# Optimization experiments

Hardware: AMD Instinct MI355X
Metric: run time of the kernel (lower is better)

Reference implementation:

```python
import jax, jax.numpy as jnp
import numpy as np

T, D, H, B = 2048, 1152, 16, 8
DH = D // H  # 72


def _apply_rope(x, cos_h, sin_h):
    # x: [T, H, DH]; cos_h, sin_h: [T, DH//2] (already chunked halves)
    c = jnp.concatenate([cos_h, cos_h], axis=-1)[:, None, :]  # [T,1,DH]
    s = jnp.concatenate([sin_h, sin_h], axis=-1)[:, None, :]
    x1, x2 = jnp.split(x, 2, axis=-1)
    rot = jnp.concatenate([-x2, x1], axis=-1)
    return x * c + rot * s


def setup_inputs() -> dict:
    key = jax.random.key(0)
    ks = jax.random.split(key, 12)
    hidden_states = jax.random.normal(ks[0], (T, D), jnp.float32)
    inner = jnp.sort(jax.random.randint(ks[1], (B - 1,), 1, T))
    cu_seqlens = jnp.concatenate(
        [jnp.zeros((1,), jnp.int32), inner.astype(jnp.int32), jnp.full((1,), T, jnp.int32)])
    cos = jax.random.uniform(ks[2], (T, DH), jnp.float32, -1.0, 1.0)
    sin = jax.random.uniform(ks[3], (T, DH), jnp.float32, -1.0, 1.0)
    std = 0.02
    Wq = jax.random.normal(ks[4], (D, D), jnp.float32) * std
    Wk = jax.random.normal(ks[5], (D, D), jnp.float32) * std
    Wv = jax.random.normal(ks[6], (D, D), jnp.float32) * std
    Wo = jax.random.normal(ks[7], (D, D), jnp.float32) * std
    bq = jnp.zeros((D,), jnp.float32)
    bk = jnp.zeros((D,), jnp.float32)
    bv = jnp.zeros((D,), jnp.float32)
    bo = jnp.zeros((D,), jnp.float32)
    return {"hidden_states": hidden_states, "cu_seqlens": cu_seqlens,
            "cos": cos, "sin": sin,
            "Wq": Wq, "bq": bq, "Wk": Wk, "bk": bk,
            "Wv": Wv, "bv": bv, "Wo": Wo, "bo": bo}


def reference(hidden_states, cu_seqlens, cos, sin, Wq, bq, Wk, bk, Wv, bv, Wo, bo):
    t = hidden_states.shape[0]
    scale = DH ** -0.5
    q = (hidden_states @ Wq.T + bq).reshape(t, H, DH)
    k = (hidden_states @ Wk.T + bk).reshape(t, H, DH)
    v = (hidden_states @ Wv.T + bv).reshape(t, H, DH)
    # RoPE: cos/sin [T, DH] are chunked in half along last dim, first half used
    cos_h = cos[:, : DH // 2]
    sin_h = sin[:, : DH // 2]
    q = _apply_rope(q, cos_h, sin_h)
    k = _apply_rope(k, cos_h, sin_h)
    # segment ids from cu_seqlens -> block-diagonal (varlen) attention mask
    pos = jnp.arange(t)
    seg = jnp.searchsorted(cu_seqlens, pos, side='right') - 1  # [T]
    mask = seg[:, None] == seg[None, :]  # [T, T]
    scores = jnp.einsum('thd,shd->hts', q, k) * scale  # [H, T, T]
    scores = jnp.where(mask[None], scores, jnp.float32(-1e30))
    attn = jax.nn.softmax(scores, axis=-1)
    out = jnp.einsum('hts,shd->thd', attn, v).reshape(t, D)
    return out @ Wo.T + bo
```

## Files before the change

kernel.cpp:

```cpp
#include <hip/hip_runtime.h>

#define TT 2048
#define DM 1152
#define NHEAD 16
#define HDIM 72
#define HDP 96
#define HDV 80
#define KSPLIT 2

typedef __attribute__((ext_vector_type(8))) __bf16 bf16x8;
typedef __attribute__((ext_vector_type(4))) float f32x4;
typedef unsigned short u16;
typedef unsigned int u32;
typedef __attribute__((ext_vector_type(4))) u16 u16x4;

__device__ inline u16 f2bf(float f){
  u32 u = __builtin_bit_cast(u32, f);
  return (u16)((u + 0x7FFFu + ((u >> 16) & 1u)) >> 16);
}
__device__ inline float bf2f(u16 v){
  return __builtin_bit_cast(float, ((u32)v) << 16);
}
__device__ inline bf16x8 ldb8(const u16* p){
  uint4 u = *(const uint4*)p;
  return __builtin_bit_cast(bf16x8, u);
}
__device__ inline f32x4 mfma16(bf16x8 a, bf16x8 b, f32x4 c){
  return __builtin_amdgcn_mfma_f32_16x16x32_bf16(a, b, c, 0, 0, 0);
}
__device__ inline void gload_lds16(const u16* g, u16* l){
  __builtin_amdgcn_global_load_lds(
      (const __attribute__((address_space(1))) void*)g,
      (__attribute__((address_space(3))) void*)l, 16, 0, 0);
}

__global__ void k_convert(const float* hid, const float* wq, const float* wk,
                          const float* wv, const float* wo, const int* cu,
                          u16* hb, u16* wqb, u16* wkb, u16* wvb, u16* wob,
                          u16* qhb, u16* khb, int* seg)
{
  long i = (long)blockIdx.x * blockDim.x + threadIdx.x;
  const long NHID4 = (long)TT * DM / 4;
  const long NW4 = (long)DM * DM / 4;
  const long NC4 = NHID4 + 4*NW4;
  if (i < NC4) {
    const float4* src; u16* dst; long o;
    if (i < NHID4) { src = (const float4*)hid; dst = hb; o = i; }
    else {
      long j = i - NHID4;
      int w = (int)(j / NW4);
      o = j - (long)w * NW4;
      src = (const float4*)((w==0)?wq:(w==1)?wk:(w==2)?wv:wo);
      dst = (w==0)?wqb:(w==1)?wkb:(w==2)?wvb:wob;
    }
    float4 v = src[o];
    u16x4 r; r.x = f2bf(v.x); r.y = f2bf(v.y); r.z = f2bf(v.z); r.w = f2bf(v.w);
    *(u16x4*)(dst + o*4) = r;
  } else {
    long j = i - NC4;
    const long PER = (long)NHEAD*TT*12;
    if (j < 2*PER) {
      int arr = (int)(j / PER);
      long r = j - (long)arr*PER;
      long th = r / 12;
      int c = (int)(r - th*12);
      ((u32*)(arr ? khb : qhb))[th*48 + 36 + c] = 0u;
    }
  }
  if (i < TT) {
    int c = 0;
    for (int e = 0; e < 9; ++e) c += (cu[e] <= (int)i);
    seg[i] = c - 1;
  }
}

__device__ __forceinline__ void gemm_m128n64(const u16* __restrict__ A,
                                             const u16* __restrict__ W,
                                             const float* __restrict__ bias,
                                             void* out, int mode, float oscale)
{
  __shared__ __align__(16) u16 As[2][128*32];
  __shared__ __align__(16) u16 Bs[2][64*32];
  int tid = threadIdx.x;
  int lane = tid & 63, wid = tid >> 6;
  int l15 = lane & 15, quad = lane >> 4;
  int bm = blockIdx.x * 128, bn = blockIdx.y * 64;
  int wm = wid*32;
  f32x4 acc[2][4] = {};
  const u16* ga = A + (long)(bm + (tid>>2))*DM + (tid&3)*8;
  const u16* gb = W + (long)(bn + (tid>>2))*DM + (tid&3)*8;
  {
    u16* lA = As[0] + wid*512; u16* lB = Bs[0] + wid*512;
    gload_lds16(ga,          lA);
    gload_lds16(ga + 64*DM,  lA + 2048);
    gload_lds16(gb,          lB);
  }
  int cur = 0;
  for (int k0 = 0; k0 < DM; k0 += 32, cur ^= 1) {
    __syncthreads();
    if (k0 + 32 < DM) {
      u16* lA = As[cur^1] + wid*512; u16* lB = Bs[cur^1] + wid*512;
      gload_lds16(ga + k0 + 32,          lA);
      gload_lds16(ga + k0 + 32 + 64*DM,  lA + 2048);
      gload_lds16(gb + k0 + 32,          lB);
    }
    bf16x8 af[2], bfr[4];
    for (int i=0;i<2;i++) af[i]  = ldb8(As[cur] + (wm + i*16 + l15)*32 + quad*8);
    for (int i=0;i<4;i++) bfr[i] = ldb8(Bs[cur] + (i*16 + l15)*32 + quad*8);
    for (int mi=0;mi<2;mi++)
      for (int ni=0;ni<4;ni++)
        acc[mi][ni] = mfma16(af[mi], bfr[ni], acc[mi][ni]);
  }
  for (int ni=0;ni<4;ni++){
    int n = bn + ni*16 + l15;
    float bv_ = bias[n];
    int h = n / HDIM, dh = n - (n / HDIM)*HDIM;
    for (int mi=0;mi<2;mi++){
      int m0 = bm + wm + mi*16 + quad*4;
      for (int r=0;r<4;r++){
        float v = (acc[mi][ni][r] + bv_) * oscale;
        int m = m0 + r;
        if (mode == 0) {
          ((u16*)out)[((long)(h*TT + m))*HDP + dh] = f2bf(v);
        } else {
          ((u16*)out)[((long)(h*HDV + dh))*TT + m] = f2bf(v);
        }
      }
    }
  }
}

__global__ __launch_bounds__(256, 4) void k_gemm_qkv(const u16* __restrict__ A,
    const u16* __restrict__ Wq, const u16* __restrict__ Wk, const u16* __restrict__ Wv,
    const float* __restrict__ bq, const float* __restrict__ bk, const float* __restrict__ bv,
    u16* oq, u16* ok, u16* ov)
{
  const float scale = 0.11785113019775793f;
  int z = blockIdx.z;
  if (z == 0)      gemm_m128n64(A, Wq, bq, oq, 0, scale);
  else if (z == 1) gemm_m128n64(A, Wk, bk, ok, 0, 1.0f);
  else             gemm_m128n64(A, Wv, bv, ov, 2, 1.0f);
}

__global__ __launch_bounds__(256, 4) void k_gemm_o(const u16* __restrict__ A,
    const u16* __restrict__ W, const float* __restrict__ bias, float* out)
{
  __shared__ __align__(16) u16 As[2][64*32];
  __shared__ __align__(16) u16 Bs[2][64*32];
  int tid = threadIdx.x;
  int lane = tid & 63, wid = tid >> 6;
  int l15 = lane & 15, quad = lane >> 4;
  int bm = blockIdx.x * 64, bn = blockIdx.y * 64;
  int wm = (wid>>1)*32, wn = (wid&1)*32;
  f32x4 acc[2][2] = {};
  const u16* ga = A + (long)(bm + (tid>>2))*DM + (tid&3)*8;
  const u16* gb = W + (long)(bn + (tid>>2))*DM + (tid&3)*8;
  {
    gload_lds16(ga, As[0] + wid*512);
    gload_lds16(gb, Bs[0] + wid*512);
  }
  int cur = 0;
  for (int k0 = 0; k0 < DM; k0 += 32, cur ^= 1) {
    __syncthreads();
    if (k0 + 32 < DM) {
      gload_lds16(ga + k0 + 32, As[cur^1] + wid*512);
      gload_lds16(gb + k0 + 32, Bs[cur^1] + wid*512);
    }
    bf16x8 af[2], bfr[2];
    for (int i=0;i<2;i++) af[i]  = ldb8(As[cur] + (wm + i*16 + l15)*32 + quad*8);
    for (int i=0;i<2;i++) bfr[i] = ldb8(Bs[cur] + (wn + i*16 + l15)*32 + quad*8);
    for (int mi=0;mi<2;mi++)
      for (int ni=0;ni<2;ni++)
        acc[mi][ni] = mfma16(af[mi], bfr[ni], acc[mi][ni]);
  }
  for (int ni=0;ni<2;ni++){
    int n = bn + wn + ni*16 + l15;
    float bv_ = bias[n];
    for (int mi=0;mi<2;mi++){
      int m0 = bm + wm + mi*16 + quad*4;
      for (int r=0;r<4;r++)
        out[(long)(m0 + r)*DM + n] = acc[mi][ni][r] + bv_;
    }
  }
}

__global__ void k_rope(u16* qh, u16* kh, const float* __restrict__ cosb,
                       const float* __restrict__ sinb)
{
  int i = blockIdx.x * blockDim.x + threadIdx.x;
  const int total = 2 * NHEAD * TT * 36;
  if (i >= total) return;
  int d = i % 36; int rest = i / 36;
  int t = rest % TT; rest /= TT;
  int h = rest % NHEAD; int qk = rest / NHEAD;
  u16* base = (qk ? kh : qh) + ((long)h*TT + t)*HDP;
  float x1 = bf2f(base[d]), x2 = bf2f(base[d+36]);
  float c = cosb[t*HDIM + d], s = sinb[t*HDIM + d];
  base[d]    = f2bf(x1*c - x2*s);
  base[d+36] = f2bf(x2*c + x1*s);
}

__global__ __launch_bounds__(256, 2) void k_attn(const u16* __restrict__ qh,
                                                 const u16* __restrict__ kh,
                                                 const u16* __restrict__ vT,
                                                 const int* __restrict__ seg,
                                                 const int* __restrict__ cu,
                                                 float* __restrict__ pacc,
                                                 float* __restrict__ plsum)
{
  __shared__ __align__(16) u16 pbuf[4][16][144];
  int h = blockIdx.y;
  int z = blockIdx.z;
  int tid = threadIdx.x, lane = tid & 63, wid = tid >> 6;
  int l15 = lane & 15, quad = lane >> 4;
  int qb0 = blockIdx.x * 128;
  int qbase = qb0 + wid*32;

  bf16x8 qf[2][3];
  int lo[2][4], hi[2][4];
  for (int t=0;t<2;t++){
    const u16* qp = qh + ((long)h*TT + qbase + t*16 + l15)*HDP + quad*8;
    qf[t][0] = ldb8(qp); qf[t][1] = ldb8(qp+32); qf[t][2] = ldb8(qp+64);
    for (int r=0;r<4;r++){
      int sq = seg[qbase + t*16 + quad*4 + r];
      lo[t][r] = cu[sq]; hi[t][r] = cu[sq+1];
    }
  }
  f32x4 acc[2][5] = {};
  float lsum[2][4] = {};

  int s_begin = cu[seg[qb0]] & ~63;
  int s_end = cu[seg[qb0 + 127] + 1];
  int nt = (s_end - s_begin + 63) >> 6;
  int nt0 = (nt + 1) >> 1;
  int it_lo = z ? nt0 : 0;
  int it_hi = z ? nt : nt0;

  const u16* kbase = kh + (long)h*TT*HDP;
  const u16* vbase = vT + ((long)h*HDV + l15)*TT + quad*8;

  if (it_lo < it_hi) {
    bf16x8 kf[4][3];
    {
      const u16* kp = kbase + (long)(s_begin + it_lo*64 + l15)*HDP + quad*8;
      for (int j=0;j<4;j++)
        for (int c=0;c<3;c++)
          kf[j][c] = ldb8(kp + j*16*HDP + c*32);
    }
    for (int it = it_lo; it < it_hi; ++it) {
      int s0 = s_begin + it*64;
      f32x4 sc[2][4] = {};
      for (int j=0;j<4;j++){
        sc[0][j] = mfma16(qf[0][0], kf[j][0], sc[0][j]);
        sc[1][j] = mfma16(qf[1][0], kf[j][0], sc[1][j]);
        sc[0][j] = mfma16(qf[0][1], kf[j][1], sc[0][j]);
        sc[1][j] = mfma16(qf[1][1], kf[j][1], sc[1][j]);
        sc[0][j] = mfma16(qf[0][2], kf[j][2], sc[0][j]);
        sc[1][j] = mfma16(qf[1][2], kf[j][2], sc[1][j]);
      }
      const u16* vp = vbase + s0;
      bf16x8 vf[5][2];
      for (int n=0;n<5;n++){
        vf[n][0] = ldb8(vp + (long)n*16*TT);
        vf[n][1] = ldb8(vp + (long)n*16*TT + 32);
      }
      if (it + 1 < it_hi) {
        const u16* kp = kbase + (long)(s0 + 64 + l15)*HDP + quad*8;
        for (int j=0;j<4;j++)
          for (int c=0;c<3;c++)
            kf[j][c] = ldb8(kp + j*16*HDP + c*32);
      }
      for (int t=0;t<2;t++){
        for (int j=0;j<4;j++){
          int kidx = s0 + j*16 + l15;
          for (int r=0;r<4;r++){
            bool in = (kidx >= lo[t][r]) && (kidx < hi[t][r]);
            float p = in ? __expf(sc[t][j][r]) : 0.f;
            lsum[t][r] += p;
            pbuf[wid][quad*4+r][t*72 + j*16 + l15] = f2bf(p);
          }
        }
      }
      bf16x8 pf[2][2];
      for (int t=0;t<2;t++){
        pf[t][0] = ldb8(&pbuf[wid][l15][t*72 + quad*8]);
        pf[t][1] = ldb8(&pbuf[wid][l15][t*72 + 32 + quad*8]);
      }
      for (int n=0;n<5;n++){
        acc[0][n] = mfma16(pf[0][0], vf[n][0], acc[0][n]);
        acc[1][n] = mfma16(pf[1][0], vf[n][0], acc[1][n]);
        acc[0][n] = mfma16(pf[0][1], vf[n][1], acc[0][n]);
        acc[1][n] = mfma16(pf[1][1], vf[n][1], acc[1][n]);
      }
    }
  }
  for (int off=1; off<16; off<<=1)
    for (int t=0;t<2;t++)
      for (int r=0;r<4;r++)
        lsum[t][r] += __shfl_xor(lsum[t][r], off, 64);
  for (int t=0;t<2;t++){
    for (int n=0;n<5;n++){
      int dh = n*16 + l15;
      for (int r=0;r<4;r++){
        int tk = qbase + t*16 + quad*4 + r;
        pacc[(((long)z*TT + tk)*NHEAD + h)*HDV + dh] = acc[t][n][r];
      }
    }
    if (l15 == 0){
      for (int r=0;r<4;r++){
        int tk = qbase + t*16 + quad*4 + r;
        plsum[((long)z*TT + tk)*NHEAD + h] = lsum[t][r];
      }
    }
  }
}

__global__ void k_combine(const float* __restrict__ pacc,
                          const float* __restrict__ plsum,
                          u16* __restrict__ ao)
{
  int i = blockIdx.x*blockDim.x + threadIdx.x;
  const int total = TT*NHEAD*HDIM;
  if (i >= total) return;
  int dh = i % HDIM; int rest = i / HDIM;
  int h = rest % NHEAD; int t = rest / NHEAD;
  long i0 = ((long)t*NHEAD + h)*HDV + dh;
  float a = pacc[i0] + pacc[(long)TT*NHEAD*HDV + i0];
  float l = plsum[t*NHEAD + h] + plsum[TT*NHEAD + t*NHEAD + h];
  ao[(long)t*DM + h*HDIM + dh] = f2bf(a / l);
}

extern "C" void kernel_launch(void* const* d_in, const int* in_sizes, int n_in,
                              void* d_out, int out_size, void* d_ws, size_t ws_size,
                              hipStream_t stream)
{
  const float* hid  = (const float*)d_in[0];
  const int*   cu   = (const int*)d_in[1];
  const float* cosb = (const float*)d_in[2];
  const float* sinb = (const float*)d_in[3];
  const float* wq   = (const float*)d_in[4];
  const float* bq   = (const float*)d_in[5];
  const float* wk   = (const float*)d_in[6];
  const float* bk   = (const float*)d_in[7];
  const float* wv   = (const float*)d_in[8];
  const float* bv   = (const float*)d_in[9];
  const float* wo   = (const float*)d_in[10];
  const float* bo   = (const float*)d_in[11];

  char* ws = (char*)d_ws;
  u16* hb  = (u16*)ws; ws += (long)TT*DM*2;
  u16* wqb = (u16*)ws; ws += (long)DM*DM*2;
  u16* wkb = (u16*)ws; ws += (long)DM*DM*2;
  u16* wvb = (u16*)ws; ws += (long)DM*DM*2;
  u16* wob = (u16*)ws; ws += (long)DM*DM*2;
  u16* qhb = (u16*)ws; ws += (long)NHEAD*TT*HDP*2;
  u16* khb = (u16*)ws; ws += (long)NHEAD*TT*HDP*2;
  u16* vTb = (u16*)ws; ws += (long)NHEAD*HDV*TT*2;
  u16* aob = (u16*)ws; ws += (long)TT*DM*2;
  int* seg = (int*)ws; ws += (long)TT*4;
  float* pacc  = (float*)ws; ws += (long)KSPLIT*TT*NHEAD*HDV*4;
  float* plsum = (float*)ws; ws += (long)KSPLIT*TT*NHEAD*4;

  long nconv = ((long)TT*DM + 4L*DM*DM)/4 + 2L*NHEAD*TT*12;
  k_convert<<<dim3((nconv + 255)/256), 256, 0, stream>>>(
      hid, wq, wk, wv, wo, cu, hb, wqb, wkb, wvb, wob, qhb, khb, seg);

  dim3 gqkv(TT/128, DM/64, 3);
  k_gemm_qkv<<<gqkv, 256, 0, stream>>>(hb, wqb, wkb, wvb, bq, bk, bv, qhb, khb, vTb);

  int nrope = 2*NHEAD*TT*36;
  k_rope<<<dim3((nrope + 255)/256), 256, 0, stream>>>(qhb, khb, cosb, sinb);

  dim3 ga(TT/128, NHEAD, KSPLIT);
  k_attn<<<ga, 256, 0, stream>>>(qhb, khb, vTb, seg, cu, pacc, plsum);

  int ncomb = TT*NHEAD*HDIM;
  k_combine<<<dim3((ncomb + 255)/256), 256, 0, stream>>>(pacc, plsum, aob);

  dim3 go(TT/64, DM/64);
  k_gemm_o<<<go, 256, 0, stream>>>(aob, wob, bo, (float*)d_out);
}
```

Baseline: 195.3 us.

## Fuse split-K attention combine into last-arriving block; reuse 128x64 GEMM for output projection

The separate combine kernel is removed. Each attention block now does a threadfence and an atomic counter increment, and the last split block for a tile sums the partial accumulators and normalizes them into the bf16 attention output. The counters are zeroed inside the rope kernel. The output projection now reuses the shared 128x64 GEMM routine with a new fp32 store mode instead of its own 64x64 kernel. This saves one launch and a pass over the partials, at the cost of atomics and a serialized tail in attention blocks, and it halves the number of output-GEMM blocks.

After: 256.2 us. 31.2% more time.

```diff
diff --git a/kernel.cpp b/kernel.cpp
--- a/kernel.cpp
+++ b/kernel.cpp
@@ -122,8 +122,10 @@
         int m = m0 + r;
         if (mode == 0) {
           ((u16*)out)[((long)(h*TT + m))*HDP + dh] = f2bf(v);
+        } else if (mode == 2) {
+          ((u16*)out)[((long)(h*HDV + dh))*TT + m] = f2bf(v);
         } else {
-          ((u16*)out)[((long)(h*HDV + dh))*TT + m] = f2bf(v);
+          ((float*)out)[(long)m*DM + n] = v;
         }
       }
     }
@@ -145,49 +147,14 @@
 __global__ __launch_bounds__(256, 4) void k_gemm_o(const u16* __restrict__ A,
     const u16* __restrict__ W, const float* __restrict__ bias, float* out)
 {
-  __shared__ __align__(16) u16 As[2][64*32];
-  __shared__ __align__(16) u16 Bs[2][64*32];
-  int tid = threadIdx.x;
-  int lane = tid & 63, wid = tid >> 6;
-  int l15 = lane & 15, quad = lane >> 4;
-  int bm = blockIdx.x * 64, bn = blockIdx.y * 64;
-  int wm = (wid>>1)*32, wn = (wid&1)*32;
-  f32x4 acc[2][2] = {};
-  const u16* ga = A + (long)(bm + (tid>>2))*DM + (tid&3)*8;
-  const u16* gb = W + (long)(bn + (tid>>2))*DM + (tid&3)*8;
-  {
-    gload_lds16(ga, As[0] + wid*512);
-    gload_lds16(gb, Bs[0] + wid*512);
-  }
-  int cur = 0;
-  for (int k0 = 0; k0 < DM; k0 += 32, cur ^= 1) {
-    __syncthreads();
-    if (k0 + 32 < DM) {
-      gload_lds16(ga + k0 + 32, As[cur^1] + wid*512);
-      gload_lds16(gb + k0 + 32, Bs[cur^1] + wid*512);
-    }
-    bf16x8 af[2], bfr[2];
-    for (int i=0;i<2;i++) af[i]  = ldb8(As[cur] + (wm + i*16 + l15)*32 + quad*8);
-    for (int i=0;i<2;i++) bfr[i] = ldb8(Bs[cur] + (wn + i*16 + l15)*32 + quad*8);
-    for (int mi=0;mi<2;mi++)
-      for (int ni=0;ni<2;ni++)
-        acc[mi][ni] = mfma16(af[mi], bfr[ni], acc[mi][ni]);
-  }
-  for (int ni=0;ni<2;ni++){
-    int n = bn + wn + ni*16 + l15;
-    float bv_ = bias[n];
-    for (int mi=0;mi<2;mi++){
-      int m0 = bm + wm + mi*16 + quad*4;
-      for (int r=0;r<4;r++)
-        out[(long)(m0 + r)*DM + n] = acc[mi][ni][r] + bv_;
-    }
-  }
+  gemm_m128n64(A, W, bias, out, 1, 1.0f);
 }
 
 __global__ void k_rope(u16* qh, u16* kh, const float* __restrict__ cosb,
-                       const float* __restrict__ sinb)
+                       const float* __restrict__ sinb, int* done)
 {
   int i = blockIdx.x * blockDim.x + threadIdx.x;
+  if (i < NHEAD*(TT/128)) done[i] = 0;
   const int total = 2 * NHEAD * TT * 36;
   if (i >= total) return;
   int d = i % 36; int rest = i / 36;
@@ -206,9 +173,12 @@
                                                  const int* __restrict__ seg,
                                                  const int* __restrict__ cu,
                                                  float* __restrict__ pacc,
-                                                 float* __restrict__ plsum)
+                                                 float* __restrict__ plsum,
+                                                 int* __restrict__ done,
+                                                 u16* __restrict__ ao)
 {
   __shared__ __align__(16) u16 pbuf[4][16][144];
+  __shared__ int flag;
   int h = blockIdx.y;
   int z = blockIdx.z;
   int tid = threadIdx.x, lane = tid & 63, wid = tid >> 6;
@@ -313,21 +283,33 @@
       }
     }
   }
-}
-
-__global__ void k_combine(const float* __restrict__ pacc,
-                          const float* __restrict__ plsum,
-                          u16* __restrict__ ao)
-{
-  int i = blockIdx.x*blockDim.x + threadIdx.x;
-  const int total = TT*NHEAD*HDIM;
-  if (i >= total) return;
-  int dh = i % HDIM; int rest = i / HDIM;
-  int h = rest % NHEAD; int t = rest / NHEAD;
-  long i0 = ((long)t*NHEAD + h)*HDV + dh;
-  float a = pacc[i0] + pacc[(long)TT*NHEAD*HDV + i0];
-  float l = plsum[t*NHEAD + h] + plsum[TT*NHEAD + t*NHEAD + h];
-  ao[(long)t*DM + h*HDIM + dh] = f2bf(a / l);
+  __threadfence();
+  if (tid == 0) flag = atomicAdd(&done[h*(TT/128) + blockIdx.x], 1);
+  __syncthreads();
+  if (flag == KSPLIT - 1) {
+    for (int t=0;t<2;t++){
+      float inv[4];
+      for (int r=0;r<4;r++){
+        int tk = qbase + t*16 + quad*4 + r;
+        float l = 0.f;
+        for (int zz=0; zz<KSPLIT; zz++)
+          l += plsum[((long)zz*TT + tk)*NHEAD + h];
+        inv[r] = 1.0f / l;
+      }
+      for (int n=0;n<5;n++){
+        int dh = n*16 + l15;
+        if (dh < HDIM){
+          for (int r=0;r<4;r++){
+            int tk = qbase + t*16 + quad*4 + r;
+            float a = 0.f;
+            for (int zz=0; zz<KSPLIT; zz++)
+              a += pacc[(((long)zz*TT + tk)*NHEAD + h)*HDV + dh];
+            ao[(long)tk*DM + h*HDIM + dh] = f2bf(a * inv[r]);
+          }
+        }
+      }
+    }
+  }
 }
 
 extern "C" void kernel_launch(void* const* d_in, const int* in_sizes, int n_in,
@@ -360,6 +342,7 @@
   int* seg = (int*)ws; ws += (long)TT*4;
   float* pacc  = (float*)ws; ws += (long)KSPLIT*TT*NHEAD*HDV*4;
   float* plsum = (float*)ws; ws += (long)KSPLIT*TT*NHEAD*4;
+  int* done = (int*)ws; ws += (long)NHEAD*(TT/128)*4;
 
   long nconv = ((long)TT*DM + 4L*DM*DM)/4 + 2L*NHEAD*TT*12;
   k_convert<<<dim3((nconv + 255)/256), 256, 0, stream>>>(
@@ -369,14 +352,11 @@
   k_gemm_qkv<<<gqkv, 256, 0, stream>>>(hb, wqb, wkb, wvb, bq, bk, bv, qhb, khb, vTb);
 
   int nrope = 2*NHEAD*TT*36;
-  k_rope<<<dim3((nrope + 255)/256), 256, 0, stream>>>(qhb, khb, cosb, sinb);
+  k_rope<<<dim3((nrope + 255)/256), 256, 0, stream>>>(qhb, khb, cosb, sinb, done);
 
   dim3 ga(TT/128, NHEAD, KSPLIT);
-  k_attn<<<ga, 256, 0, stream>>>(qhb, khb, vTb, seg, cu, pacc, plsum);
-
-  int ncomb = TT*NHEAD*HDIM;
-  k_combine<<<dim3((ncomb + 255)/256), 256, 0, stream>>>(pacc, plsum, aob);
-
-  dim3 go(TT/64, DM/64);
+  k_attn<<<ga, 256, 0, stream>>>(qhb, khb, vTb, seg, cu, pacc, plsum, done, aob);
+
+  dim3 go(TT/128, DM/64);
   k_gemm_o<<<go, 256, 0, stream>>>(aob, wob, bo, (float*)d_out);
 }
```
